# Kernel optimization log

Hardware: AMD Instinct MI355X
Metric: run time of the kernel (lower is better)

Reference implementation:

```python
import jax, jax.numpy as jnp
import numpy as np

B, L, D, F = 1, 4096, 4096, 11008
# (start, end, side): side 0 = vision expert, side 1 = language expert.
# Mirrors merge_section_size over alternating contiguous vision/language token ranges.
SEGMENTS = [(0, 1024, 0), (1024, 2048, 1), (2048, 3072, 0), (3072, 4096, 1)]


def setup_inputs() -> dict:
    key = jax.random.key(0)
    ks = jax.random.split(key, 7)
    s = 0.02  # weight init scale
    hidden_states = jax.random.normal(ks[0], (B, L, D), jnp.float32)
    tt = np.zeros((B, L), np.int32)
    for a, b, side in SEGMENTS:
        tt[:, a:b] = side
    token_type_ids = jnp.asarray(tt)
    lg_w = jax.random.normal(ks[1], (D, F), jnp.float32) * s
    lu_w = jax.random.normal(ks[2], (D, F), jnp.float32) * s
    ld_w = jax.random.normal(ks[3], (F, D), jnp.float32) * s
    vg_w = jax.random.normal(ks[4], (D, F), jnp.float32) * s
    vu_w = jax.random.normal(ks[5], (D, F), jnp.float32) * s
    vd_w = jax.random.normal(ks[6], (F, D), jnp.float32) * s
    return {
        'hidden_states': hidden_states,
        'token_type_ids': token_type_ids,
        'lg_w': lg_w, 'lu_w': lu_w, 'ld_w': ld_w,
        'vg_w': vg_w, 'vu_w': vu_w, 'vd_w': vd_w,
    }


def _swiglu_mlp(x, gw, uw, dw):
    # x: [B, T, D] -> [B, T, D]; down(silu(gate(x)) * up(x))
    h = jax.nn.silu(jnp.einsum('btd,df->btf', x, gw)) * jnp.einsum('btd,df->btf', x, uw)
    return jnp.einsum('btf,fd->btd', h, dw)


def reference(hidden_states, token_type_ids, lg_w, lu_w, ld_w, vg_w, vu_w, vd_w):
    # Split-dispatch over static contiguous segments, then concat along seq dim.
    outs = []
    for a, b, side in SEGMENTS:
        seg = hidden_states[:, a:b, :]
        if side == 1:
            outs.append(_swiglu_mlp(seg, lg_w, lu_w, ld_w))
        else:
            outs.append(_swiglu_mlp(seg, vg_w, vu_w, vd_w))
    return jnp.concatenate(outs, axis=1)
```

## Files before the change

kernel.cpp:

```cpp
#include <hip/hip_runtime.h>
#include <math.h>

typedef unsigned short u16;
typedef short s16x8 __attribute__((ext_vector_type(8)));
typedef float f32x4 __attribute__((ext_vector_type(4)));

#define GLOAD16(gp, lp)                                                        \
  __builtin_amdgcn_global_load_lds(                                            \
      (const __attribute__((address_space(1))) void*)(gp),                     \
      (__attribute__((address_space(3))) void*)(lp), 16, 0, 0)

__device__ __forceinline__ u16 f2bf(float f) {
  union { float f; unsigned u; } v; v.f = f;
  unsigned r = v.u + 0x7fffu + ((v.u >> 16) & 1u);
  return (u16)(r >> 16);
}

__global__ __launch_bounds__(256) void cvt_x_kernel(const float* __restrict__ in,
                                                    u16* __restrict__ out) {
  size_t i = ((size_t)blockIdx.x * 256 + threadIdx.x) * 8;
  float4 a = *(const float4*)(in + i);
  float4 b = *(const float4*)(in + i + 4);
  s16x8 v;
  v[0] = (short)f2bf(a.x); v[1] = (short)f2bf(a.y);
  v[2] = (short)f2bf(a.z); v[3] = (short)f2bf(a.w);
  v[4] = (short)f2bf(b.x); v[5] = (short)f2bf(b.y);
  v[6] = (short)f2bf(b.z); v[7] = (short)f2bf(b.w);
  *(s16x8*)(out + i) = v;
}

__global__ __launch_bounds__(256) void transpose_cvt_kernel(
    const float* __restrict__ in0, const float* __restrict__ in1,
    const float* __restrict__ in2, const float* __restrict__ in3,
    const float* __restrict__ in4, const float* __restrict__ in5,
    u16* __restrict__ o01, u16* __restrict__ o23,
    u16* __restrict__ o4, u16* __restrict__ o5) {
  __shared__ float s[64 * 65];
  const int mat = blockIdx.y;
  const float* in; u16* out;
  switch (mat) {
    case 0: in = in0; out = o01; break;
    case 1: in = in1; out = o01; break;
    case 2: in = in2; out = o23; break;
    case 3: in = in3; out = o23; break;
    case 4: in = in4; out = o4; break;
    default: in = in5; out = o5; break;
  }
  const int R = (mat < 4) ? 4096 : 11008;
  const int C = (mat < 4) ? 11008 : 4096;
  const int nTc = C >> 6;
  const int tr = blockIdx.x / nTc, tc = blockIdx.x - tr * nTc;
  const int r0 = tr << 6, c0 = tc << 6;
  const int t = threadIdx.x;
#pragma unroll
  for (int p = 0; p < 4; ++p) {
    const int lr = p * 16 + (t >> 4);
    const int lc = (t & 15) * 4;
    float4 v = *(const float4*)(in + (size_t)(r0 + lr) * C + (c0 + lc));
    float* sp = &s[lr * 65 + lc];
    sp[0] = v.x; sp[1] = v.y; sp[2] = v.z; sp[3] = v.w;
  }
  __syncthreads();
#pragma unroll
  for (int q = 0; q < 2; ++q) {
    const int oc = q * 32 + (t >> 3);
    const int orr = (t & 7) * 8;
    s16x8 v;
#pragma unroll
    for (int i = 0; i < 8; ++i) v[i] = (short)f2bf(s[(orr + i) * 65 + oc]);
    const int f = c0 + oc;
    size_t orow;
    if (mat < 4) orow = (size_t)((f >> 4) << 5) + ((mat & 1) << 4) + (f & 15);
    else         orow = (size_t)f;
    *(s16x8*)(out + orow * R + (r0 + orr)) = v;
  }
}

template <int KB, int EPI>
__global__ __launch_bounds__(512, 1) void gemm256(
    const u16* __restrict__ A, const u16* __restrict__ Bl,
    const u16* __restrict__ Bv, const int* __restrict__ tt,
    void* __restrict__ OutP) {
  constexpr int NK = KB / 128;
  constexpr int L = NK / 2;
  __shared__ u16 sA[2][2][128][64];
  __shared__ u16 sB[2][2][128][64];

  const int nwg = gridDim.x;
  const int bid = blockIdx.x;
  const int wg = (bid & 7) * (nwg >> 3) + (bid >> 3);
  const int mT = wg & 15;
  const int nT = wg >> 4;

  const int t = threadIdx.x;
  const int lane = t & 63;
  const int rlo = lane & 15;
  const int hi = lane >> 4;
  const int wn = (t >> 6) & 3;
  const int wm = (t >> 8) & 1;

  const int side = tt[mT << 8];
  const u16* B = side ? Bl : Bv;

  const int rowq = t >> 3;
  const int gsw = ((t & 7) ^ (rowq & 7)) << 4;
  const char* srcA = (const char*)A + (size_t)(mT * 256 + rowq) * KB + gsw;
  const char* srcB = (const char*)B + (size_t)(nT * 256 + rowq) * KB + gsw;
  char* ldsA = (char*)&sA[0][0][0][0];
  char* ldsB = (char*)&sB[0][0][0][0];
  const int woff = (t & 448) << 4;

#define STG_A(d, h, kt)                                                        \
  do {                                                                         \
    GLOAD16(srcA + (size_t)((h) * 128) * KB + (kt) * 128,                      \
            ldsA + (d) * 32768 + (h) * 16384 + woff);                          \
    GLOAD16(srcA + (size_t)((h) * 128 + 64) * KB + (kt) * 128,                 \
            ldsA + (d) * 32768 + (h) * 16384 + 8192 + woff);                   \
  } while (0)
#define STG_B(d, h, kt)                                                        \
  do {                                                                         \
    GLOAD16(srcB + (size_t)((h) * 128) * KB + (kt) * 128,                      \
            ldsB + (d) * 32768 + (h) * 16384 + woff);                          \
    GLOAD16(srcB + (size_t)((h) * 128 + 64) * KB + (kt) * 128,                 \
            ldsB + (d) * 32768 + (h) * 16384 + 8192 + woff);                   \
  } while (0)

  const int cxa = (hi ^ (rlo & 7)) << 4;
  const int cxb = ((4 + hi) ^ (rlo & 7)) << 4;
  const int arow = (wm * 64 + rlo) * 128;
  const int brow = (wn * 32 + rlo) * 128;

  s16x8 af[4][2], bf[2][2];
  f32x4 acc[8][4];
  const f32x4 z = {0.f, 0.f, 0.f, 0.f};
#pragma unroll
  for (int i = 0; i < 8; ++i)
#pragma unroll
    for (int j = 0; j < 4; ++j) acc[i][j] = z;

#define LDA(d, mh)                                                             \
  do {                                                                         \
    _Pragma("unroll") for (int fi = 0; fi < 4; ++fi) {                         \
      const char* p = ldsA + (d) * 32768 + (mh) * 16384 + arow + fi * 2048;    \
      af[fi][0] = *(const s16x8*)(p + cxa);                                    \
      af[fi][1] = *(const s16x8*)(p + cxb);                                    \
    }                                                                          \
  } while (0)
#define LDB(d, nh)                                                             \
  do {                                                                         \
    _Pragma("unroll") for (int gi = 0; gi < 2; ++gi) {                         \
      const char* p = ldsB + (d) * 32768 + (nh) * 16384 + brow + gi * 2048;    \
      bf[gi][0] = *(const s16x8*)(p + cxa);                                    \
      bf[gi][1] = *(const s16x8*)(p + cxb);                                    \
    }                                                                          \
  } while (0)
#define MFMA16(mh, nh)                                                         \
  do {                                                                         \
    __builtin_amdgcn_s_setprio(1);                                             \
    _Pragma("unroll") for (int fi = 0; fi < 4; ++fi)                           \
        _Pragma("unroll") for (int gi = 0; gi < 2; ++gi) {                     \
      acc[(mh)*4 + fi][(nh)*2 + gi] = __builtin_amdgcn_mfma_f32_16x16x32_bf16( \
          af[fi][0], bf[gi][0], acc[(mh)*4 + fi][(nh)*2 + gi], 0, 0, 0);       \
      acc[(mh)*4 + fi][(nh)*2 + gi] = __builtin_amdgcn_mfma_f32_16x16x32_bf16( \
          af[fi][1], bf[gi][1], acc[(mh)*4 + fi][(nh)*2 + gi], 0, 0, 0);       \
    }                                                                          \
    __builtin_amdgcn_s_setprio(0);                                             \
  } while (0)
#define SBAR() __builtin_amdgcn_s_barrier()
#define VMCNT4() do { asm volatile("s_waitcnt vmcnt(4)" ::: "memory");         \
                      __builtin_amdgcn_sched_barrier(0); } while (0)
#define VMCNT0() do { asm volatile("s_waitcnt vmcnt(0)" ::: "memory");         \
                      __builtin_amdgcn_sched_barrier(0); } while (0)

  STG_A(0, 0, 0); STG_A(0, 1, 0); STG_B(0, 0, 0); STG_B(0, 1, 0);
  STG_B(1, 0, 1); STG_A(1, 1, 1);
  VMCNT4();
  SBAR();

  for (int it = 0; it < L - 1; ++it) {
    const int T = 2 * it;
    LDA(0, 0); LDB(0, 0);
    STG_A(1, 0, T + 1); STG_B(1, 1, T + 1);
    SBAR(); MFMA16(0, 0); SBAR();
    LDA(0, 1);
    SBAR(); MFMA16(1, 0); SBAR();
    LDB(0, 1);
    STG_B(0, 0, T + 2);
    SBAR(); MFMA16(1, 1); SBAR();
    LDA(0, 0);
    STG_A(0, 1, T + 2);
    SBAR(); MFMA16(0, 1);
    VMCNT4(); SBAR();
    LDA(1, 0); LDB(1, 0);
    STG_A(0, 0, T + 2); STG_B(0, 1, T + 2);
    SBAR(); MFMA16(0, 0); SBAR();
    LDA(1, 1);
    SBAR(); MFMA16(1, 0); SBAR();
    LDB(1, 1);
    STG_B(1, 0, T + 3);
    SBAR(); MFMA16(1, 1); SBAR();
    LDA(1, 0);
    STG_A(1, 1, T + 3);
    SBAR(); MFMA16(0, 1);
    VMCNT4(); SBAR();
  }
  {
    const int T = NK - 2;
    LDA(0, 0); LDB(0, 0);
    STG_A(1, 0, T + 1); STG_B(1, 1, T + 1);
    SBAR(); MFMA16(0, 0); SBAR();
    LDA(0, 1);
    SBAR(); MFMA16(1, 0); SBAR();
    LDB(0, 1);
    SBAR(); MFMA16(1, 1); SBAR();
    LDA(0, 0);
    SBAR(); MFMA16(0, 1);
    VMCNT0(); SBAR();
    LDA(1, 0); LDB(1, 0);
    SBAR(); MFMA16(0, 0); SBAR();
    LDA(1, 1);
    SBAR(); MFMA16(1, 0); SBAR();
    LDB(1, 1);
    SBAR(); MFMA16(1, 1); SBAR();
    LDA(1, 0);
    SBAR(); MFMA16(0, 1);
  }

  if (EPI == 0) {
    u16* H = (u16*)OutP;
#pragma unroll
    for (int mh = 0; mh < 2; ++mh)
#pragma unroll
      for (int fi = 0; fi < 4; ++fi) {
        const int row0 = mT * 256 + mh * 128 + wm * 64 + fi * 16 + hi * 4;
#pragma unroll
        for (int nh = 0; nh < 2; ++nh) {
          const int fc = nT * 128 + (nh * 4 + wn) * 16 + rlo;
          const f32x4 g = acc[mh * 4 + fi][nh * 2 + 0];
          const f32x4 u = acc[mh * 4 + fi][nh * 2 + 1];
#pragma unroll
          for (int r = 0; r < 4; ++r) {
            const float gv = g[r];
            const float hv = gv / (1.f + __expf(-gv)) * u[r];
            H[(size_t)(row0 + r) * 11008 + fc] = f2bf(hv);
          }
        }
      }
  } else {
    float* O = (float*)OutP;
#pragma unroll
    for (int mh = 0; mh < 2; ++mh)
#pragma unroll
      for (int fi = 0; fi < 4; ++fi) {
        const int row0 = mT * 256 + mh * 128 + wm * 64 + fi * 16 + hi * 4;
#pragma unroll
        for (int nh = 0; nh < 2; ++nh)
#pragma unroll
          for (int gi = 0; gi < 2; ++gi) {
            const int col = nT * 256 + nh * 128 + wn * 32 + gi * 16 + rlo;
            const f32x4 a = acc[mh * 4 + fi][nh * 2 + gi];
#pragma unroll
            for (int r = 0; r < 4; ++r)
              O[(size_t)(row0 + r) * 4096 + col] = a[r];
          }
      }
  }
#undef STG_A
#undef STG_B
#undef LDA
#undef LDB
#undef MFMA16
#undef SBAR
#undef VMCNT4
#undef VMCNT0
}

extern "C" void kernel_launch(void* const* d_in, const int* in_sizes, int n_in,
                              void* d_out, int out_size, void* d_ws, size_t ws_size,
                              hipStream_t stream) {
  (void)in_sizes; (void)n_in; (void)out_size; (void)ws_size;
  const float* x  = (const float*)d_in[0];
  const int*   tt = (const int*)d_in[1];
  const float* lg = (const float*)d_in[2];
  const float* lu = (const float*)d_in[3];
  const float* ld = (const float*)d_in[4];
  const float* vg = (const float*)d_in[5];
  const float* vu = (const float*)d_in[6];
  const float* vd = (const float*)d_in[7];

  u16* ws  = (u16*)d_ws;
  u16* xbf = ws;
  u16* GUl = xbf + 16777216;
  u16* GUv = GUl + 90177536;
  u16* ldT = GUv + 90177536;
  u16* vdT = ldT + 45088768;
  u16* hbuf = vdT + 45088768;

  cvt_x_kernel<<<dim3(8192), dim3(256), 0, stream>>>(x, xbf);
  transpose_cvt_kernel<<<dim3(11008, 6), dim3(256), 0, stream>>>(
      lg, lu, vg, vu, ld, vd, GUl, GUv, ldT, vdT);
  gemm256<8192, 0><<<dim3(1376), dim3(512), 0, stream>>>(xbf, GUl, GUv, tt, hbuf);
  gemm256<22016, 1><<<dim3(256), dim3(512), 0, stream>>>(hbuf, ldT, vdT, tt, d_out);
}
```

Before: 1.520 ms.

## Rebalance global-to-LDS staging across MFMA phases with explicit lgkmcnt waits

Spreads the global_load_lds staging calls evenly over the four MFMA sub-phases of each K step, one stage per phase instead of clustered pairs. It loosens the vmcnt wait from 4 to 6 to allow deeper in-flight loads, and adds explicit lgkmcnt waits before each MFMA block. The sched_barrier fences around the vmcnt waits are removed. The goal is to smooth memory issue and overlap loads with MFMA, at the cost of more wait instructions and a risk of hazards if the counter values do not match the actual number of outstanding ops.

```diff
diff --git a/kernel.cpp b/kernel.cpp
--- a/kernel.cpp
+++ b/kernel.cpp
@@ -167,63 +167,69 @@
     __builtin_amdgcn_s_setprio(0);                                             \
   } while (0)
 #define SBAR() __builtin_amdgcn_s_barrier()
-#define VMCNT4() do { asm volatile("s_waitcnt vmcnt(4)" ::: "memory");         \
-                      __builtin_amdgcn_sched_barrier(0); } while (0)
-#define VMCNT0() do { asm volatile("s_waitcnt vmcnt(0)" ::: "memory");         \
-                      __builtin_amdgcn_sched_barrier(0); } while (0)
-
-  STG_A(0, 0, 0); STG_A(0, 1, 0); STG_B(0, 0, 0); STG_B(0, 1, 0);
-  STG_B(1, 0, 1); STG_A(1, 1, 1);
-  VMCNT4();
+#define LGKM0() asm volatile("s_waitcnt lgkmcnt(0)")
+#define LGKM8() asm volatile("s_waitcnt lgkmcnt(8)")
+#define VMCNT6() asm volatile("s_waitcnt vmcnt(6)")
+#define VMCNT0() asm volatile("s_waitcnt vmcnt(0)")
+
+  STG_A(0, 0, 0); STG_B(0, 0, 0); STG_A(0, 1, 0); STG_B(0, 1, 0);
+  STG_B(1, 0, 1); STG_A(1, 1, 1); STG_B(1, 1, 1);
+  VMCNT6();
   SBAR();
 
   for (int it = 0; it < L - 1; ++it) {
     const int T = 2 * it;
     LDA(0, 0); LDB(0, 0);
-    STG_A(1, 0, T + 1); STG_B(1, 1, T + 1);
-    SBAR(); MFMA16(0, 0); SBAR();
+    STG_A(1, 0, T + 1);
+    LGKM8();
+    SBAR(); LGKM0(); MFMA16(0, 0); SBAR();
     LDA(0, 1);
-    SBAR(); MFMA16(1, 0); SBAR();
+    STG_B(0, 0, T + 2);
+    SBAR(); LGKM0(); MFMA16(1, 0); SBAR();
     LDB(0, 1);
-    STG_B(0, 0, T + 2);
-    SBAR(); MFMA16(1, 1); SBAR();
+    STG_A(0, 1, T + 2);
+    SBAR(); LGKM0(); MFMA16(1, 1); SBAR();
     LDA(0, 0);
-    STG_A(0, 1, T + 2);
-    SBAR(); MFMA16(0, 1);
-    VMCNT4(); SBAR();
+    STG_B(0, 1, T + 2);
+    VMCNT6();
+    SBAR(); LGKM0(); MFMA16(0, 1); SBAR();
     LDA(1, 0); LDB(1, 0);
-    STG_A(0, 0, T + 2); STG_B(0, 1, T + 2);
-    SBAR(); MFMA16(0, 0); SBAR();
+    STG_A(0, 0, T + 2);
+    LGKM8();
+    SBAR(); LGKM0(); MFMA16(0, 0); SBAR();
     LDA(1, 1);
-    SBAR(); MFMA16(1, 0); SBAR();
+    STG_B(1, 0, T + 3);
+    SBAR(); LGKM0(); MFMA16(1, 0); SBAR();
     LDB(1, 1);
-    STG_B(1, 0, T + 3);
-    SBAR(); MFMA16(1, 1); SBAR();
+    STG_A(1, 1, T + 3);
+    SBAR(); LGKM0(); MFMA16(1, 1); SBAR();
     LDA(1, 0);
-    STG_A(1, 1, T + 3);
-    SBAR(); MFMA16(0, 1);
-    VMCNT4(); SBAR();
+    STG_B(1, 1, T + 3);
+    VMCNT6();
+    SBAR(); LGKM0(); MFMA16(0, 1); SBAR();
   }
   {
     const int T = NK - 2;
     LDA(0, 0); LDB(0, 0);
-    STG_A(1, 0, T + 1); STG_B(1, 1, T + 1);
-    SBAR(); MFMA16(0, 0); SBAR();
+    STG_A(1, 0, T + 1);
+    LGKM8();
+    SBAR(); LGKM0(); MFMA16(0, 0); SBAR();
     LDA(0, 1);
-    SBAR(); MFMA16(1, 0); SBAR();
+    SBAR(); LGKM0(); MFMA16(1, 0); SBAR();
     LDB(0, 1);
-    SBAR(); MFMA16(1, 1); SBAR();
+    SBAR(); LGKM0(); MFMA16(1, 1); SBAR();
     LDA(0, 0);
-    SBAR(); MFMA16(0, 1);
-    VMCNT0(); SBAR();
+    VMCNT0();
+    SBAR(); LGKM0(); MFMA16(0, 1); SBAR();
     LDA(1, 0); LDB(1, 0);
-    SBAR(); MFMA16(0, 0); SBAR();
+    LGKM8();
+    SBAR(); LGKM0(); MFMA16(0, 0); SBAR();
     LDA(1, 1);
-    SBAR(); MFMA16(1, 0); SBAR();
+    SBAR(); LGKM0(); MFMA16(1, 0); SBAR();
     LDB(1, 1);
-    SBAR(); MFMA16(1, 1); SBAR();
+    SBAR(); LGKM0(); MFMA16(1, 1); SBAR();
     LDA(1, 0);
-    SBAR(); MFMA16(0, 1);
+    SBAR(); LGKM0(); MFMA16(0, 1);
   }
 
   if (EPI == 0) {
@@ -271,7 +277,9 @@
 #undef LDB
 #undef MFMA16
 #undef SBAR
-#undef VMCNT4
+#undef LGKM0
+#undef LGKM8
+#undef VMCNT6
 #undef VMCNT0
 }
 
```

Result: faster. 1.474 ms (-3.0%).
